# Optimization experiments

Measured on AMD Instinct MI355X. Metric: run time of the kernel, lower is better.

The kernel has to match this reference:

```python
import jax, jax.numpy as jnp
import numpy as np

B, N, DIM, H, DH = 2, 2048, 1024, 16, 64
INNER = H * DH
EPS = 1e-12  # F.normalize eps
MAX_LOG_SCALE = np.log(1.0 / 0.01)  # clamp max for logit_scale


def setup_inputs() -> dict:
    key = jax.random.key(0)
    k1, k2, k3, k4 = jax.random.split(key, 4)
    x = jax.random.normal(k1, (B, N, DIM), dtype=jnp.float32)
    # Linear weights stored as [in, out] (transpose of torch's [out, in])
    w_qkv = jax.random.normal(k2, (DIM, 3 * INNER), dtype=jnp.float32) * (DIM ** -0.5)
    w_out = jax.random.normal(k3, (INNER, DIM), dtype=jnp.float32) * (INNER ** -0.5)
    b_out = jax.random.normal(k4, (DIM,), dtype=jnp.float32) * 0.01
    logit_scale = jnp.full((H, 1, 1), jnp.log(10.0), dtype=jnp.float32)
    return {"x": x, "w_qkv": w_qkv, "w_out": w_out, "b_out": b_out,
            "logit_scale": logit_scale}


def reference(x, w_qkv, w_out, b_out, logit_scale):
    b, n, dim = x.shape
    h = logit_scale.shape[0]
    qkv = x @ w_qkv                              # [b, n, 3*inner]
    q, k, v = jnp.split(qkv, 3, axis=-1)
    split_heads = lambda t: t.reshape(b, n, h, -1).transpose(0, 2, 1, 3)  # b h n d
    q, k, v = split_heads(q), split_heads(k), split_heads(v)
    # L2-normalize q and k (F.normalize semantics: divide by max(norm, eps))
    qn = q / jnp.maximum(jnp.linalg.norm(q, axis=-1, keepdims=True), EPS)
    kn = k / jnp.maximum(jnp.linalg.norm(k, axis=-1, keepdims=True), EPS)
    scale = jnp.exp(jnp.minimum(logit_scale, MAX_LOG_SCALE))  # [h,1,1], per-head temp
    cos_dots = jnp.einsum('bhid,bhjd->bhij', qn, kn) * scale   # [b,h,n,n]
    # NOTE: masking in the source mutates the unused plain-dot `dots` tensor,
    # so the output never depends on the mask -> faithfully omitted.
    attn = jax.nn.softmax(cos_dots, axis=-1)
    out = jnp.einsum('bhij,bhjd->bhid', attn, v)               # [b,h,n,d]
    out = out.transpose(0, 2, 1, 3).reshape(b, n, -1)          # [b,n,inner]
    return out @ w_out + b_out
```

## Files before the change

### kernel.cpp

```cpp
#include <hip/hip_runtime.h>

typedef __attribute__((ext_vector_type(8))) short bf16x8;
typedef __attribute__((ext_vector_type(4))) float f32x4;
typedef __attribute__((ext_vector_type(16))) float f32x16;
typedef unsigned short u16;
typedef unsigned int u32;
typedef __attribute__((ext_vector_type(4))) unsigned int u32x4;

#define DEV static __device__ __forceinline__

DEV u16 f2bf(float f) {
  u32 u = __float_as_uint(f);
  u += 0x7FFFu + ((u >> 16) & 1u);
  return (u16)(u >> 16);
}
DEV float bf2f(u16 h) { return __uint_as_float(((u32)h) << 16); }

DEV void gload16(const void* g, void* l) {
  __builtin_amdgcn_global_load_lds((const __attribute__((address_space(1))) void*)g,
                                   (__attribute__((address_space(3))) void*)l, 16, 0, 0);
}

#define MFMA16(a, b, c) __builtin_amdgcn_mfma_f32_16x16x32_bf16((a), (b), (c), 0, 0, 0)
#define MFMA32(a, b, c) __builtin_amdgcn_mfma_f32_32x32x16_bf16((a), (b), (c), 0, 0, 0)

DEV u32 cvtpk(float lo, float hi) {
  u32 r;
  asm("v_cvt_pk_bf16_f32 %0, %1, %2" : "=v"(r) : "v"(lo), "v"(hi));
  return r;
}
DEV void plswap(u32& a, u32& b) {
  asm volatile("v_permlane32_swap_b32 %0, %1" : "+v"(a), "+v"(b));
}
DEV bf16x8 asbf(u32x4 v) {
  union { u32x4 u; bf16x8 b; } x;
  x.u = v;
  return x.b;
}

DEV void rawbar() {
  __builtin_amdgcn_sched_barrier(0);
  asm volatile("" ::: "memory");
  __builtin_amdgcn_s_barrier();
  asm volatile("" ::: "memory");
  __builtin_amdgcn_sched_barrier(0);
}
#define VMCNT4() asm volatile("s_waitcnt vmcnt(4)" ::: "memory")
#define VMCNT0() asm volatile("s_waitcnt vmcnt(0)" ::: "memory")

#define MAXLOG 4.6051701859880914f

__global__ __launch_bounds__(256) void k_prep(const float* __restrict__ x,
                                              u16* __restrict__ Xbf,
                                              const float* __restrict__ w_qkv,
                                              u16* __restrict__ Wqkvt,
                                              const float* __restrict__ w_out,
                                              u16* __restrict__ Woutt) {
  __shared__ u16 lds[64][72];
  int blk = blockIdx.x;
  int t = threadIdx.x;
  if (blk < 2048) {
    int i = blk * 256 + t;
    const f32x4* p = (const f32x4*)(x + (size_t)i * 8);
    f32x4 a = p[0], b = p[1];
    bf16x8 o;
    o[0] = (short)f2bf(a[0]); o[1] = (short)f2bf(a[1]);
    o[2] = (short)f2bf(a[2]); o[3] = (short)f2bf(a[3]);
    o[4] = (short)f2bf(b[0]); o[5] = (short)f2bf(b[1]);
    o[6] = (short)f2bf(b[2]); o[7] = (short)f2bf(b[3]);
    *(bf16x8*)(Xbf + (size_t)i * 8) = o;
    return;
  }
  const float* src;
  u16* dst;
  int rows, cols, bx, by;
  if (blk < 2816) {
    int q = blk - 2048;
    src = w_qkv; dst = Wqkvt; rows = 1024; cols = 3072;
    bx = q % 48; by = q / 48;
  } else {
    int q = blk - 2816;
    src = w_out; dst = Woutt; rows = 1024; cols = 1024;
    bx = q % 16; by = q / 16;
  }
  int r0 = by * 64, c0 = bx * 64;
  int r = t >> 2, cq = (t & 3) << 4;
  const float* s = src + (size_t)(r0 + r) * cols + c0 + cq;
#pragma unroll
  for (int i = 0; i < 16; i += 4) {
    f32x4 v = *(const f32x4*)(s + i);
    lds[r][cq + i + 0] = f2bf(v[0]);
    lds[r][cq + i + 1] = f2bf(v[1]);
    lds[r][cq + i + 2] = f2bf(v[2]);
    lds[r][cq + i + 3] = f2bf(v[3]);
  }
  __syncthreads();
  int c = t >> 2, rq = (t & 3) << 4;
  bf16x8 o0, o1;
#pragma unroll
  for (int i = 0; i < 8; ++i) o0[i] = (short)lds[rq + i][c];
#pragma unroll
  for (int i = 0; i < 8; ++i) o1[i] = (short)lds[rq + 8 + i][c];
  u16* d = dst + (size_t)(c0 + c) * rows + r0 + rq;
  *(bf16x8*)d = o0;
  *(bf16x8*)(d + 8) = o1;
}

template <bool OUT_BF16, bool HAS_BIAS>
__global__ __launch_bounds__(256) void k_gemm_bt(const u16* __restrict__ A,
                                                 const u16* __restrict__ Bt,
                                                 void* __restrict__ Cout,
                                                 const float* __restrict__ bias,
                                                 int M, int N, int K, int nbx) {
  __shared__ __align__(16) u16 lsA[128 * 32];
  __shared__ __align__(16) u16 lsB[128 * 32];
  int tid = threadIdx.x;
  int lane = tid & 63, wave = tid >> 6;
  int wr = (wave >> 1) * 64, wc = (wave & 1) * 64;
  int nwg = gridDim.x;
  int orig = blockIdx.x;
  int wg = (orig & 7) * (nwg >> 3) + (orig >> 3);
  int bm = (wg / nbx) * 128, bn = (wg % nbx) * 128;

  f32x4 acc[4][4] = {};

  const u16* aSrc[2]; u16* aDst[2];
  const u16* bSrc[2]; u16* bDst[2];
#pragma unroll
  for (int j = 0; j < 2; ++j) {
    int s = wave * 128 + j * 64 + lane;
    int row = s >> 2, chunk = s & 3;
    int g = chunk ^ ((row >> 1) & 3);
    aSrc[j] = A + (size_t)(bm + row) * K + g * 8;
    bSrc[j] = Bt + (size_t)(bn + row) * K + g * 8;
    aDst[j] = &lsA[(wave * 128 + j * 64) * 8];
    bDst[j] = &lsB[(wave * 128 + j * 64) * 8];
  }

  for (int k0 = 0; k0 < K; k0 += 32) {
    __syncthreads();
    gload16(aSrc[0] + k0, aDst[0]);
    gload16(aSrc[1] + k0, aDst[1]);
    gload16(bSrc[0] + k0, bDst[0]);
    gload16(bSrc[1] + k0, bDst[1]);
    __syncthreads();
    bf16x8 af[4], bfr[4];
#pragma unroll
    for (int m = 0; m < 4; ++m) {
      int r = wr + m * 16 + (lane & 15);
      int p = (lane >> 4) ^ ((r >> 1) & 3);
      af[m] = *(const bf16x8*)&lsA[r * 32 + p * 8];
    }
#pragma unroll
    for (int n = 0; n < 4; ++n) {
      int r = wc + n * 16 + (lane & 15);
      int p = (lane >> 4) ^ ((r >> 1) & 3);
      bfr[n] = *(const bf16x8*)&lsB[r * 32 + p * 8];
    }
#pragma unroll
    for (int m = 0; m < 4; ++m)
#pragma unroll
      for (int n = 0; n < 4; ++n)
        acc[m][n] = MFMA16(af[m], bfr[n], acc[m][n]);
  }

#pragma unroll
  for (int m = 0; m < 4; ++m) {
    int row = bm + wr + m * 16 + ((lane >> 4) << 2);
#pragma unroll
    for (int n = 0; n < 4; ++n) {
      int col = bn + wc + n * 16 + (lane & 15);
#pragma unroll
      for (int j = 0; j < 4; ++j) {
        if (OUT_BF16) {
          ((u16*)Cout)[(size_t)(row + j) * N + col] = f2bf(acc[m][n][j]);
        } else {
          float bb = HAS_BIAS ? bias[col] : 0.f;
          ((float*)Cout)[(size_t)(row + j) * N + col] = acc[m][n][j] + bb;
        }
      }
    }
  }
}

__global__ __launch_bounds__(256) void k_qknorm(const u16* __restrict__ QKV,
                                                const float* __restrict__ logit_scale,
                                                u16* __restrict__ Qn, u16* __restrict__ Kn) {
  int idx = blockIdx.x * 256 + threadIdx.x;
  int n = idx & 2047, bh = idx >> 11;
  int b = bh >> 4, h = bh & 15;
  float scale = __expf(fminf(logit_scale[h], MAXLOG));
  const u16* qp = QKV + ((size_t)(b * 2048 + n)) * 3072 + h * 64;
  bf16x8 qv[8], kv[8];
#pragma unroll
  for (int j = 0; j < 8; ++j) {
    qv[j] = *(const bf16x8*)(qp + j * 8);
    kv[j] = *(const bf16x8*)(qp + 1024 + j * 8);
  }
  float sq = 0.f, sk = 0.f;
#pragma unroll
  for (int j = 0; j < 8; ++j)
#pragma unroll
    for (int e = 0; e < 8; ++e) {
      float fq = bf2f((u16)qv[j][e]);
      float fk = bf2f((u16)kv[j][e]);
      sq += fq * fq;
      sk += fk * fk;
    }
  float rq = scale / fmaxf(sqrtf(sq), 1e-12f);
  float rk = 1.0f / fmaxf(sqrtf(sk), 1e-12f);
  u16* qo = Qn + ((size_t)bh * 2048 + n) * 64;
  u16* ko = Kn + ((size_t)bh * 2048 + n) * 64;
#pragma unroll
  for (int j = 0; j < 8; ++j) {
    bf16x8 oq, ok;
#pragma unroll
    for (int e = 0; e < 8; ++e) {
      oq[e] = (short)f2bf(bf2f((u16)qv[j][e]) * rq);
      ok[e] = (short)f2bf(bf2f((u16)kv[j][e]) * rk);
    }
    *(bf16x8*)(qo + j * 8) = oq;
    *(bf16x8*)(ko + j * 8) = ok;
  }
}

__global__ __launch_bounds__(256) void k_vtrans(const u16* __restrict__ QKV,
                                                u16* __restrict__ Vt) {
  __shared__ u16 lds[64][72];
  int nt = blockIdx.x, h = blockIdx.y, b = blockIdx.z;
  int tid = threadIdx.x;
  int bh = b * 16 + h;
  int r = tid >> 2, cq = (tid & 3) << 4;
  size_t voff = ((size_t)(b * 2048 + nt * 64 + r)) * 3072 + 2048 + h * 64 + cq;
  *(bf16x8*)&lds[r][cq] = *(const bf16x8*)&QKV[voff];
  *(bf16x8*)&lds[r][cq + 8] = *(const bf16x8*)&QKV[voff + 8];
  __syncthreads();
  int d = tid >> 2, nq = (tid & 3) << 4;
  bf16x8 o0, o1;
#pragma unroll
  for (int i = 0; i < 8; ++i) o0[i] = (short)lds[nq + i][d];
#pragma unroll
  for (int i = 0; i < 8; ++i) o1[i] = (short)lds[nq + 8 + i][d];
  u16* vd = Vt + ((size_t)bh * 64 + d) * 2048 + nt * 64 + nq;
  *(bf16x8*)vd = o0;
  *(bf16x8*)(vd + 8) = o1;
}

__global__ __launch_bounds__(256, 2) void k_flash(const u16* __restrict__ Qn,
                                                  const u16* __restrict__ Kn,
                                                  const u16* __restrict__ Vt,
                                                  const float* __restrict__ logit_scale,
                                                  u16* __restrict__ AO) {
  __shared__ __align__(16) u16 lsK[2][64 * 64];
  __shared__ __align__(16) u16 lsV[2][64 * 64];
  __shared__ float l_s[4][32];
  int tid = threadIdx.x, lane = tid & 63, wave = tid >> 6;
  int r31 = lane & 31, h = lane >> 5;
  int bh = blockIdx.x, b = bh >> 4, hd = bh & 15;
  int qw = blockIdx.y * 128 + wave * 32;
  const u16* Q = Qn + (size_t)bh * 2048 * 64;
  const u16* Kb = Kn + (size_t)bh * 2048 * 64;
  const u16* Vb = Vt + (size_t)bh * 64 * 2048;

  float negC = -__expf(fminf(logit_scale[hd], MAXLOG));

  bf16x8 qB[4];
#pragma unroll
  for (int ks = 0; ks < 4; ++ks)
    qB[ks] = *(const bf16x8*)&Q[(size_t)(qw + r31) * 64 + ks * 16 + h * 8];

  size_t kGO[2], vGO[2];
  int lOff[2];
#pragma unroll
  for (int j = 0; j < 2; ++j) {
    int s = j * 256 + tid;
    int row = s >> 3, ch = s & 7, g = ch ^ (row & 7);
    kGO[j] = (size_t)row * 64 + g * 8;
    vGO[j] = (size_t)row * 2048 + g * 8;
    lOff[j] = s * 8;
  }

  int off[2][4];
#pragma unroll
  for (int a = 0; a < 2; ++a)
#pragma unroll
    for (int ks = 0; ks < 4; ++ks)
      off[a][ks] = (a * 32 + r31) * 64 + ((((ks << 1) | h) ^ (r31 & 7)) << 3);

  f32x16 o0, o1;
#pragma unroll
  for (int i = 0; i < 16; ++i) { o0[i] = 0.f; o1[i] = 0.f; }
  float lsum = 0.f;

#define STAGE(dstbuf, kvt)                                          \
  {                                                                 \
    size_t kv0 = (size_t)(kvt) * 64;                                \
    gload16(Kb + kv0 * 64 + kGO[0], &lsK[dstbuf][lOff[0]]);         \
    gload16(Kb + kv0 * 64 + kGO[1], &lsK[dstbuf][lOff[1]]);         \
    gload16(Vb + kv0 + vGO[0], &lsV[dstbuf][lOff[0]]);              \
    gload16(Vb + kv0 + vGO[1], &lsV[dstbuf][lOff[1]]);              \
  }

  STAGE(0, 0);

#pragma unroll 1
  for (int t = 0; t < 32; ++t) {
    int cur = t & 1;
    if (t < 31) {
      STAGE(cur ^ 1, t + 1);
      VMCNT4();
    } else {
      VMCNT0();
    }
    rawbar();
    const u16* Kl = lsK[cur];
    const u16* Vl = lsV[cur];

    f32x16 s0, s1;
#pragma unroll
    for (int i = 0; i < 16; ++i) { s0[i] = negC; s1[i] = negC; }
    bf16x8 k0f[4], k1f[4];
#pragma unroll
    for (int ks = 0; ks < 4; ++ks) {
      k0f[ks] = *(const bf16x8*)&Kl[off[0][ks]];
      k1f[ks] = *(const bf16x8*)&Kl[off[1][ks]];
    }
    __builtin_amdgcn_s_setprio(1);
#pragma unroll
    for (int ks = 0; ks < 4; ++ks) {
      s0 = MFMA32(k0f[ks], qB[ks], s0);
      s1 = MFMA32(k1f[ks], qB[ks], s1);
    }
    __builtin_amdgcn_s_setprio(0);

    bf16x8 v0f[4], v1f[4];
#pragma unroll
    for (int ks = 0; ks < 4; ++ks) {
      v0f[ks] = *(const bf16x8*)&Vl[off[0][ks]];
      v1f[ks] = *(const bf16x8*)&Vl[off[1][ks]];
    }

#pragma unroll
    for (int i = 0; i < 16; ++i) {
      float e0 = __expf(s0[i]);
      float e1 = __expf(s1[i]);
      lsum += e0 + e1;
      s0[i] = e0; s1[i] = e1;
    }

    bf16x8 pa[4];
    {
      u32 c0 = cvtpk(s0[0], s0[1]),  c1 = cvtpk(s0[2], s0[3]);
      u32 c2 = cvtpk(s0[4], s0[5]),  c3 = cvtpk(s0[6], s0[7]);
      u32 c4 = cvtpk(s0[8], s0[9]),  c5 = cvtpk(s0[10], s0[11]);
      u32 c6 = cvtpk(s0[12], s0[13]), c7 = cvtpk(s0[14], s0[15]);
      plswap(c0, c2); plswap(c1, c3); plswap(c4, c6); plswap(c5, c7);
      pa[0] = asbf((u32x4){c0, c1, c2, c3});
      pa[1] = asbf((u32x4){c4, c5, c6, c7});
      u32 d0 = cvtpk(s1[0], s1[1]),  d1 = cvtpk(s1[2], s1[3]);
      u32 d2 = cvtpk(s1[4], s1[5]),  d3 = cvtpk(s1[6], s1[7]);
      u32 d4 = cvtpk(s1[8], s1[9]),  d5 = cvtpk(s1[10], s1[11]);
      u32 d6 = cvtpk(s1[12], s1[13]), d7 = cvtpk(s1[14], s1[15]);
      plswap(d0, d2); plswap(d1, d3); plswap(d4, d6); plswap(d5, d7);
      pa[2] = asbf((u32x4){d0, d1, d2, d3});
      pa[3] = asbf((u32x4){d4, d5, d6, d7});
    }

    __builtin_amdgcn_s_setprio(1);
#pragma unroll
    for (int ks = 0; ks < 4; ++ks) {
      o0 = MFMA32(pa[ks], v0f[ks], o0);
      o1 = MFMA32(pa[ks], v1f[ks], o1);
    }
    __builtin_amdgcn_s_setprio(0);

    rawbar();
  }
#undef STAGE

  float ltot = lsum + __shfl_xor(lsum, 32, 64);
  if (h == 0) l_s[wave][r31] = 1.0f / ltot;
  __syncthreads();

#pragma unroll
  for (int r = 0; r < 16; ++r) {
    int cr = (r & 3) + ((r >> 2) << 3) + (h << 2);
    int qr = qw + cr;
    float li = l_s[wave][cr];
    size_t base = ((size_t)(b * 2048 + qr)) * 1024 + hd * 64;
    AO[base + r31] = f2bf(o0[r] * li);
    AO[base + 32 + r31] = f2bf(o1[r] * li);
  }
}

extern "C" void kernel_launch(void* const* d_in, const int* in_sizes, int n_in,
                              void* d_out, int out_size, void* d_ws, size_t ws_size,
                              hipStream_t stream) {
  const float* x = (const float*)d_in[0];
  const float* w_qkv = (const float*)d_in[1];
  const float* w_out = (const float*)d_in[2];
  const float* b_out = (const float*)d_in[3];
  const float* logit_scale = (const float*)d_in[4];

  char* ws = (char*)d_ws;
  u16* Xbf   = (u16*)(ws);
  u16* Wqkvt = (u16*)(ws + (8ll << 20));
  u16* Woutt = (u16*)(ws + (14ll << 20));
  u16* QKV   = (u16*)(ws + (16ll << 20));
  u16* Qn    = (u16*)(ws + (40ll << 20));
  u16* Kn    = (u16*)(ws + (48ll << 20));
  u16* Vt    = (u16*)(ws + (56ll << 20));
  u16* AO    = Xbf;
  float* out = (float*)d_out;

  k_prep<<<3072, 256, 0, stream>>>(x, Xbf, w_qkv, Wqkvt, w_out, Woutt);
  k_gemm_bt<true, false><<<768, 256, 0, stream>>>(Xbf, Wqkvt, QKV, nullptr,
                                                  4096, 3072, 1024, 24);
  k_qknorm<<<256, 256, 0, stream>>>(QKV, logit_scale, Qn, Kn);
  k_vtrans<<<dim3(32, 16, 2), 256, 0, stream>>>(QKV, Vt);
  k_flash<<<dim3(32, 16), 256, 0, stream>>>(Qn, Kn, Vt, logit_scale, AO);
  k_gemm_bt<false, true><<<256, 256, 0, stream>>>(AO, Woutt, out, b_out,
                                                  4096, 1024, 1024, 8);
}
```

Measured before the change: 136.2 us.

## Merge qk-norm and V-transpose kernels, add smaller-tile output GEMM

Merges the q/k normalization kernel and the V transpose kernel into one launch, with the block index choosing which job each block does. This removes one kernel launch and its gap. It also replaces the output projection GEMM with a dedicated 128x64-tile kernel over 512 blocks instead of 256. The smaller tiles spread the work over more workgroups on the many-CU device, at the cost of less data reuse per tile and a simple single-buffered K loop.

```diff
diff --git a/kernel.cpp b/kernel.cpp
--- a/kernel.cpp
+++ b/kernel.cpp
@@ -183,52 +183,129 @@
   }
 }
 
-__global__ __launch_bounds__(256) void k_qknorm(const u16* __restrict__ QKV,
+__global__ __launch_bounds__(256) void k_gemm_out(const u16* __restrict__ A,
+                                                  const u16* __restrict__ Bt,
+                                                  float* __restrict__ Cout,
+                                                  const float* __restrict__ bias,
+                                                  int M, int N, int K, int nbx) {
+  __shared__ __align__(16) u16 lsA[128 * 32];
+  __shared__ __align__(16) u16 lsB[64 * 32];
+  int tid = threadIdx.x;
+  int lane = tid & 63, wave = tid >> 6;
+  int wr = (wave >> 1) * 64, wc = (wave & 1) * 32;
+  int nwg = gridDim.x;
+  int orig = blockIdx.x;
+  int wg = (orig & 7) * (nwg >> 3) + (orig >> 3);
+  int bm = (wg / nbx) * 128, bn = (wg % nbx) * 64;
+
+  f32x4 acc[4][2] = {};
+
+  const u16* aSrc[2]; u16* aDst[2];
+  const u16* bSrc;    u16* bDst;
+#pragma unroll
+  for (int j = 0; j < 2; ++j) {
+    int s = wave * 128 + j * 64 + lane;
+    int row = s >> 2, chunk = s & 3;
+    int g = chunk ^ ((row >> 1) & 3);
+    aSrc[j] = A + (size_t)(bm + row) * K + g * 8;
+    aDst[j] = &lsA[(wave * 128 + j * 64) * 8];
+  }
+  {
+    int s = wave * 64 + lane;
+    int row = s >> 2, chunk = s & 3;
+    int g = chunk ^ ((row >> 1) & 3);
+    bSrc = Bt + (size_t)(bn + row) * K + g * 8;
+    bDst = &lsB[(wave * 64) * 8];
+  }
+
+  for (int k0 = 0; k0 < K; k0 += 32) {
+    __syncthreads();
+    gload16(aSrc[0] + k0, aDst[0]);
+    gload16(aSrc[1] + k0, aDst[1]);
+    gload16(bSrc + k0, bDst);
+    __syncthreads();
+    bf16x8 af[4], bfr[2];
+#pragma unroll
+    for (int m = 0; m < 4; ++m) {
+      int r = wr + m * 16 + (lane & 15);
+      int p = (lane >> 4) ^ ((r >> 1) & 3);
+      af[m] = *(const bf16x8*)&lsA[r * 32 + p * 8];
+    }
+#pragma unroll
+    for (int n = 0; n < 2; ++n) {
+      int r = wc + n * 16 + (lane & 15);
+      int p = (lane >> 4) ^ ((r >> 1) & 3);
+      bfr[n] = *(const bf16x8*)&lsB[r * 32 + p * 8];
+    }
+#pragma unroll
+    for (int m = 0; m < 4; ++m)
+#pragma unroll
+      for (int n = 0; n < 2; ++n)
+        acc[m][n] = MFMA16(af[m], bfr[n], acc[m][n]);
+  }
+
+#pragma unroll
+  for (int m = 0; m < 4; ++m) {
+    int row = bm + wr + m * 16 + ((lane >> 4) << 2);
+#pragma unroll
+    for (int n = 0; n < 2; ++n) {
+      int col = bn + wc + n * 16 + (lane & 15);
+      float bb = bias[col];
+#pragma unroll
+      for (int j = 0; j < 4; ++j)
+        Cout[(size_t)(row + j) * N + col] = acc[m][n][j] + bb;
+    }
+  }
+}
+
+__global__ __launch_bounds__(256) void k_qkpack(const u16* __restrict__ QKV,
                                                 const float* __restrict__ logit_scale,
-                                                u16* __restrict__ Qn, u16* __restrict__ Kn) {
-  int idx = blockIdx.x * 256 + threadIdx.x;
-  int n = idx & 2047, bh = idx >> 11;
-  int b = bh >> 4, h = bh & 15;
-  float scale = __expf(fminf(logit_scale[h], MAXLOG));
-  const u16* qp = QKV + ((size_t)(b * 2048 + n)) * 3072 + h * 64;
-  bf16x8 qv[8], kv[8];
-#pragma unroll
-  for (int j = 0; j < 8; ++j) {
-    qv[j] = *(const bf16x8*)(qp + j * 8);
-    kv[j] = *(const bf16x8*)(qp + 1024 + j * 8);
-  }
-  float sq = 0.f, sk = 0.f;
-#pragma unroll
-  for (int j = 0; j < 8; ++j)
-#pragma unroll
-    for (int e = 0; e < 8; ++e) {
-      float fq = bf2f((u16)qv[j][e]);
-      float fk = bf2f((u16)kv[j][e]);
-      sq += fq * fq;
-      sk += fk * fk;
-    }
-  float rq = scale / fmaxf(sqrtf(sq), 1e-12f);
-  float rk = 1.0f / fmaxf(sqrtf(sk), 1e-12f);
-  u16* qo = Qn + ((size_t)bh * 2048 + n) * 64;
-  u16* ko = Kn + ((size_t)bh * 2048 + n) * 64;
-#pragma unroll
-  for (int j = 0; j < 8; ++j) {
-    bf16x8 oq, ok;
-#pragma unroll
-    for (int e = 0; e < 8; ++e) {
-      oq[e] = (short)f2bf(bf2f((u16)qv[j][e]) * rq);
-      ok[e] = (short)f2bf(bf2f((u16)kv[j][e]) * rk);
-    }
-    *(bf16x8*)(qo + j * 8) = oq;
-    *(bf16x8*)(ko + j * 8) = ok;
-  }
-}
-
-__global__ __launch_bounds__(256) void k_vtrans(const u16* __restrict__ QKV,
+                                                u16* __restrict__ Qn, u16* __restrict__ Kn,
                                                 u16* __restrict__ Vt) {
   __shared__ u16 lds[64][72];
-  int nt = blockIdx.x, h = blockIdx.y, b = blockIdx.z;
+  int blk = blockIdx.x;
   int tid = threadIdx.x;
+  if (blk < 256) {
+    int idx = blk * 256 + tid;
+    int n = idx & 2047, bh = idx >> 11;
+    int b = bh >> 4, h = bh & 15;
+    float scale = __expf(fminf(logit_scale[h], MAXLOG));
+    const u16* qp = QKV + ((size_t)(b * 2048 + n)) * 3072 + h * 64;
+    bf16x8 qv[8], kv[8];
+#pragma unroll
+    for (int j = 0; j < 8; ++j) {
+      qv[j] = *(const bf16x8*)(qp + j * 8);
+      kv[j] = *(const bf16x8*)(qp + 1024 + j * 8);
+    }
+    float sq = 0.f, sk = 0.f;
+#pragma unroll
+    for (int j = 0; j < 8; ++j)
+#pragma unroll
+      for (int e = 0; e < 8; ++e) {
+        float fq = bf2f((u16)qv[j][e]);
+        float fk = bf2f((u16)kv[j][e]);
+        sq += fq * fq;
+        sk += fk * fk;
+      }
+    float rq = scale / fmaxf(sqrtf(sq), 1e-12f);
+    float rk = 1.0f / fmaxf(sqrtf(sk), 1e-12f);
+    u16* qo = Qn + ((size_t)bh * 2048 + n) * 64;
+    u16* ko = Kn + ((size_t)bh * 2048 + n) * 64;
+#pragma unroll
+    for (int j = 0; j < 8; ++j) {
+      bf16x8 oq, ok;
+#pragma unroll
+      for (int e = 0; e < 8; ++e) {
+        oq[e] = (short)f2bf(bf2f((u16)qv[j][e]) * rq);
+        ok[e] = (short)f2bf(bf2f((u16)kv[j][e]) * rk);
+      }
+      *(bf16x8*)(qo + j * 8) = oq;
+      *(bf16x8*)(ko + j * 8) = ok;
+    }
+    return;
+  }
+  int q = blk - 256;
+  int nt = q & 31, h = (q >> 5) & 15, b = q >> 9;
   int bh = b * 16 + h;
   int r = tid >> 2, cq = (tid & 3) << 4;
   size_t voff = ((size_t)(b * 2048 + nt * 64 + r)) * 3072 + 2048 + h * 64 + cq;
@@ -416,9 +493,8 @@
   k_prep<<<3072, 256, 0, stream>>>(x, Xbf, w_qkv, Wqkvt, w_out, Woutt);
   k_gemm_bt<true, false><<<768, 256, 0, stream>>>(Xbf, Wqkvt, QKV, nullptr,
                                                   4096, 3072, 1024, 24);
-  k_qknorm<<<256, 256, 0, stream>>>(QKV, logit_scale, Qn, Kn);
-  k_vtrans<<<dim3(32, 16, 2), 256, 0, stream>>>(QKV, Vt);
+  k_qkpack<<<1280, 256, 0, stream>>>(QKV, logit_scale, Qn, Kn, Vt);
   k_flash<<<dim3(32, 16), 256, 0, stream>>>(Qn, Kn, Vt, logit_scale, AO);
-  k_gemm_bt<false, true><<<256, 256, 0, stream>>>(AO, Woutt, out, b_out,
-                                                  4096, 1024, 1024, 8);
-}
+  k_gemm_out<<<512, 256, 0, stream>>>(AO, Woutt, out, b_out,
+                                      4096, 1024, 1024, 16);
+}
```

Measured after the change: 128.7 us. 5.5% less time.
